# Performance work log

Measured on AMD Instinct MI355X. Metric: run time of the kernel, lower is better.

Reference implementation:

```python
import jax, jax.numpy as jnp
import numpy as np

B, S, D, H = 4, 2048, 512, 8
DK = D // H


def setup_inputs() -> dict:
    key = jax.random.key(0)
    ks = jax.random.split(key, 8)
    std = 1.0 / np.sqrt(D)
    return {
        "query": jax.random.normal(ks[0], (B, S, D), jnp.float32),
        "key": jax.random.normal(ks[1], (B, S, D), jnp.float32),
        "value": jax.random.normal(ks[2], (B, S, D), jnp.float32),
        "Wq": jax.random.normal(ks[3], (D, D), jnp.float32) * std,
        "Wk": jax.random.normal(ks[4], (D, D), jnp.float32) * std,
        "Wv": jax.random.normal(ks[5], (D, D), jnp.float32) * std,
        "Wo": jax.random.normal(ks[6], (D, D), jnp.float32) * std,
        "bo": jnp.zeros((D,), jnp.float32),
    }


def reference(query, key, value, Wq, Wk, Wv, Wo, bo):
    # nn.Linear stores weight [out, in]; y = x @ W.T
    def split_heads(x):  # [B,S,D] -> [B,H,S,DK]
        return x.reshape(B, S, H, DK).transpose(0, 2, 1, 3)

    Q = split_heads(query @ Wq.T)
    K = split_heads(key @ Wk.T)
    V = split_heads(value @ Wv.T)
    scale = jnp.sqrt(jnp.asarray(DK, Q.dtype))
    scores = jnp.einsum("bhqd,bhkd->bhqk", Q, K) / scale  # [B,H,S,S]
    attn = jax.nn.softmax(scores, axis=-1)  # dropout=0 / eval mode
    ctx = jnp.einsum("bhqk,bhkd->bhqd", attn, V)
    ctx = ctx.transpose(0, 2, 1, 3).reshape(B, S, D)
    return ctx @ Wo.T + bo
```

## Files before the change

### kernel.cpp

```cpp
#include <hip/hip_runtime.h>
#include <hip/hip_bf16.h>
#include <stdint.h>

#define DEV __device__ __forceinline__

typedef __attribute__((ext_vector_type(8))) __bf16 bf16x8;
typedef __attribute__((ext_vector_type(4))) float f32x4;
typedef __attribute__((ext_vector_type(16))) float f32x16;
typedef __attribute__((ext_vector_type(4))) short short4v;
typedef __attribute__((ext_vector_type(8))) short short8v;
typedef __attribute__((ext_vector_type(4))) unsigned int uint4v;

constexpr int B_ = 4, S_ = 2048, D_ = 512, H_ = 8, DK_ = 64;
constexpr int M_ = B_ * S_;
constexpr int K_ = D_;

DEV unsigned short f2bf(float f) {
  unsigned int u = __builtin_bit_cast(unsigned int, f);
  unsigned int r = (u + 0x7fffu + ((u >> 16) & 1u)) >> 16;
  return (unsigned short)r;
}

DEV void gld16(const void* g, void* l) {
  __builtin_amdgcn_global_load_lds(
      (const __attribute__((address_space(1))) unsigned int*)g,
      (__attribute__((address_space(3))) unsigned int*)l, 16, 0, 0);
}

DEV f32x4 mfma16(bf16x8 a, bf16x8 b, f32x4 c) {
  return __builtin_amdgcn_mfma_f32_16x16x32_bf16(a, b, c, 0, 0, 0);
}
DEV f32x16 mfma32(bf16x8 a, bf16x8 b, f32x16 c) {
  return __builtin_amdgcn_mfma_f32_32x32x16_bf16(a, b, c, 0, 0, 0);
}

DEV short4v tr16(const void* p) {
  short4v d;
  asm volatile("ds_read_b64_tr_b16 %0, %1"
               : "=v"(d)
               : "v"((const __attribute__((address_space(3))) char*)p));
  return d;
}

DEV unsigned pkbf(float a, float b) {
  unsigned r;
  asm("v_cvt_pk_bf16_f32 %0, %1, %2" : "=v"(r) : "v"(a), "v"(b));
  return r;
}

DEV void pl32swap(unsigned& a, unsigned& b) {
  asm volatile("v_permlane32_swap_b32 %0, %1" : "+v"(a), "+v"(b));
}

__global__ __launch_bounds__(256) void convert_all(
    const float* __restrict__ q, const float* __restrict__ k, const float* __restrict__ v,
    const float* __restrict__ wq, const float* __restrict__ wk,
    const float* __restrict__ wv, const float* __restrict__ wo,
    unsigned short* __restrict__ xq, unsigned short* __restrict__ xk,
    unsigned short* __restrict__ xv, unsigned short* __restrict__ wqb,
    unsigned short* __restrict__ wkb, unsigned short* __restrict__ wvb,
    unsigned short* __restrict__ wob)
{
  constexpr int NX = M_ * D_;
  constexpr int NW = D_ * D_;
  constexpr int TOT = (3 * NX + 4 * NW) / 4;
  for (int u = blockIdx.x * blockDim.x + threadIdx.x; u < TOT;
       u += gridDim.x * blockDim.x) {
    int e = u * 4;
    const float* src; unsigned short* dst; int off;
    if (e < 3 * NX) {
      int t = e >> 22; off = e & (NX - 1);
      src = (t == 0) ? q : ((t == 1) ? k : v);
      dst = (t == 0) ? xq : ((t == 1) ? xk : xv);
    } else {
      int e2 = e - 3 * NX;
      int t = e2 >> 18; off = e2 & (NW - 1);
      src = (t == 0) ? wq : ((t == 1) ? wk : ((t == 2) ? wv : wo));
      dst = (t == 0) ? wqb : ((t == 1) ? wkb : ((t == 2) ? wvb : wob));
    }
    float4 f = *(const float4*)(src + off);
    short4v o;
    o.x = (short)f2bf(f.x); o.y = (short)f2bf(f.y);
    o.z = (short)f2bf(f.z); o.w = (short)f2bf(f.w);
    *(short4v*)(dst + off) = o;
  }
}

template <int MODE>
__global__ __launch_bounds__(256, 2) void gemm_bt(
    const unsigned short* __restrict__ A, const unsigned short* __restrict__ W,
    unsigned short* __restrict__ outH, float* __restrict__ outF,
    const float* __restrict__ bias)
{
  constexpr int BM = 128, BN = 64, BK = 64, NKT = K_ / BK;
  __shared__ unsigned short As[2][BM * BK];
  __shared__ unsigned short Bs[2][BN * BK];
  const int tid = threadIdx.x, lane = tid & 63, wave = tid >> 6;
  const int bn0 = blockIdx.x * BN, bm0 = blockIdx.y * BM;
  const int wr = (wave >> 1) * 64, wc = (wave & 1) * 32;
  const int frow = lane & 15, fk16 = (lane >> 4) * 16;

  f32x4 acc[4][2];
#pragma unroll
  for (int i = 0; i < 4; ++i)
#pragma unroll
    for (int j = 0; j < 2; ++j)
#pragma unroll
      for (int r = 0; r < 4; ++r) acc[i][j][r] = 0.f;

  auto stage = [&](int kt, int buf) {
#pragma unroll
    for (int i = 0; i < 4; ++i) {
      int o = (wave * 4 + i) * 1024;
      int ol = o + lane * 16;
      int src = ol ^ (((ol >> 7) & 7) << 4);
      gld16((const char*)A + (size_t)(bm0 + (src >> 7)) * (K_ * 2) + kt * 128 + (src & 127),
            (char*)As[buf] + o);
    }
#pragma unroll
    for (int i = 0; i < 2; ++i) {
      int o = (wave * 2 + i) * 1024;
      int ol = o + lane * 16;
      int src = ol ^ (((ol >> 7) & 7) << 4);
      gld16((const char*)W + (size_t)(bn0 + (src >> 7)) * (K_ * 2) + kt * 128 + (src & 127),
            (char*)Bs[buf] + o);
    }
  };

  stage(0, 0);
  __syncthreads();
  int cur = 0;
  for (int kt = 0; kt < NKT; ++kt) {
    if (kt + 1 < NKT) stage(kt + 1, cur ^ 1);
#pragma unroll
    for (int kc = 0; kc < 2; ++kc) {
      bf16x8 a[4], b[2];
#pragma unroll
      for (int i = 0; i < 4; ++i) {
        int row = wr + i * 16 + frow;
        a[i] = *(const bf16x8*)((const char*)As[cur] +
                ((row * 128 + kc * 64 + fk16) ^ ((row & 7) << 4)));
      }
#pragma unroll
      for (int j = 0; j < 2; ++j) {
        int row = wc + j * 16 + frow;
        b[j] = *(const bf16x8*)((const char*)Bs[cur] +
                ((row * 128 + kc * 64 + fk16) ^ ((row & 7) << 4)));
      }
      __builtin_amdgcn_s_setprio(1);
#pragma unroll
      for (int i = 0; i < 4; ++i)
#pragma unroll
        for (int j = 0; j < 2; ++j)
          acc[i][j] = mfma16(a[i], b[j], acc[i][j]);
      __builtin_amdgcn_s_setprio(0);
    }
    __syncthreads();
    cur ^= 1;
  }

  const int r0 = (lane >> 4) * 4, cn = lane & 15;
#pragma unroll
  for (int i = 0; i < 4; ++i)
#pragma unroll
    for (int j = 0; j < 2; ++j)
#pragma unroll
      for (int r = 0; r < 4; ++r) {
        int gm = bm0 + wr + i * 16 + r0 + r;
        int gn = bn0 + wc + j * 16 + cn;
        float val = acc[i][j][r];
        if (MODE == 0) {
          int bb = gm >> 11, ss = gm & (S_ - 1), hh = gn >> 6, dk = gn & 63;
          outH[((size_t)(bb * H_ + hh) * S_ + ss) * DK_ + dk] = f2bf(val);
        } else {
          outF[(size_t)gm * D_ + gn] = val + bias[gn];
        }
      }
}

__global__ __launch_bounds__(256, 2) void attn(
    const unsigned short* __restrict__ Qb, const unsigned short* __restrict__ Kb,
    const unsigned short* __restrict__ Vb, unsigned short* __restrict__ Ctx)
{
  constexpr int QB = 128, KVB = 64, NT = S_ / KVB;
  __shared__ unsigned short Qs[QB * DK_];
  __shared__ unsigned short Kd[2][KVB * DK_];
  __shared__ unsigned short Vd[2][KVB * DK_];
  __shared__ float smA[4][32];
  const int tid = threadIdx.x, lane = tid & 63, wave = tid >> 6;
  const int hi = lane >> 5, l31 = lane & 31, g1 = (lane >> 4) & 1;
  const int bh = blockIdx.y, q0 = blockIdx.x * QB;
  const size_t hb = (size_t)bh * S_ * DK_;
  const char* Qg = (const char*)(Qb + hb + (size_t)q0 * DK_);
  const char* Kg = (const char*)(Kb + hb);
  const char* Vg = (const char*)(Vb + hb);

  auto stageSwz = [&](const char* gbase, unsigned short* lds, int o) {
    int ol = o + lane * 16;
    int src = ol ^ (((ol >> 7) & 7) << 4);
    gld16(gbase + src, (char*)lds + o);
  };
  auto stageVt = [&](const char* gbase, unsigned short* lds, int o) {
    int ol = o + lane * 16;
    int E0 = ol >> 1;
    int st = E0 >> 6, rr = (E0 >> 4) & 3, c0 = E0 & 15;
    int kk = (st >> 2) * 4 + rr, dd = (st & 3) * 16 + c0;
    gld16(gbase + (kk * DK_ + dd) * 2, (char*)lds + o);
  };

#pragma unroll
  for (int i = 0; i < 4; ++i) stageSwz(Qg, Qs, (wave * 4 + i) * 1024);
#pragma unroll
  for (int i = 0; i < 2; ++i) stageSwz(Kg, Kd[0], (wave * 2 + i) * 1024);
#pragma unroll
  for (int i = 0; i < 2; ++i) stageVt(Vg, Vd[0], (wave * 2 + i) * 1024);
  __syncthreads();

  bf16x8 qf[4];
  {
    int row = wave * 32 + l31;
    int rb = row * 128, sw = (row & 7) << 4;
#pragma unroll
    for (int c = 0; c < 4; ++c)
      qf[c] = *(const bf16x8*)((const char*)Qs + ((rb + c * 32 + hi * 16) ^ sw));
  }

  f32x16 oacc[2];
#pragma unroll
  for (int dt = 0; dt < 2; ++dt)
#pragma unroll
    for (int r = 0; r < 16; ++r) oacc[dt][r] = 0.f;
  float m2 = -1e30f, lsum = 0.f;
  constexpr float SCL2 = 0.125f * 1.44269504089f;

  int cur = 0;
  for (int t = 0; t < NT; ++t) {
    if (t + 1 < NT) {
      const char* Kg1 = Kg + (size_t)(t + 1) * (KVB * DK_ * 2);
      const char* Vg1 = Vg + (size_t)(t + 1) * (KVB * DK_ * 2);
#pragma unroll
      for (int i = 0; i < 2; ++i) stageSwz(Kg1, Kd[cur ^ 1], (wave * 2 + i) * 1024);
#pragma unroll
      for (int i = 0; i < 2; ++i) stageVt(Vg1, Vd[cur ^ 1], (wave * 2 + i) * 1024);
    }

    f32x16 sacc[2];
#pragma unroll
    for (int k2 = 0; k2 < 2; ++k2)
#pragma unroll
      for (int r = 0; r < 16; ++r) sacc[k2][r] = 0.f;
    __builtin_amdgcn_s_setprio(1);
#pragma unroll
    for (int c = 0; c < 4; ++c) {
#pragma unroll
      for (int k2 = 0; k2 < 2; ++k2) {
        int row = k2 * 32 + l31;
        bf16x8 kf = *(const bf16x8*)((const char*)Kd[cur] +
                     ((row * 128 + c * 32 + hi * 16) ^ ((row & 7) << 4)));
        sacc[k2] = mfma32(kf, qf[c], sacc[k2]);
      }
    }
    __builtin_amdgcn_s_setprio(0);

    float mloc = sacc[0][0];
#pragma unroll
    for (int k2 = 0; k2 < 2; ++k2)
#pragma unroll
      for (int r = 0; r < 16; ++r) mloc = fmaxf(mloc, sacc[k2][r]);
    mloc = fmaxf(mloc, __shfl_xor(mloc, 32));
    float m2n = fmaxf(m2, mloc * SCL2);
    float alpha = __builtin_amdgcn_exp2f(m2 - m2n);
    m2 = m2n;
    float psum = 0.f;
#pragma unroll
    for (int k2 = 0; k2 < 2; ++k2)
#pragma unroll
      for (int r = 0; r < 16; ++r) {
        float p = __builtin_amdgcn_exp2f(fmaf(sacc[k2][r], SCL2, -m2n));
        sacc[k2][r] = p;
        psum += p;
      }
    psum += __shfl_xor(psum, 32);
    lsum = lsum * alpha + psum;

    if (lane < 32) smA[wave][lane] = alpha;
    f32x4 av[4];
#pragma unroll
    for (int s = 0; s < 4; ++s)
      av[s] = *(const f32x4*)&smA[wave][s * 8 + hi * 4];
#pragma unroll
    for (int dt = 0; dt < 2; ++dt)
#pragma unroll
      for (int r = 0; r < 16; ++r) oacc[dt][r] *= av[r >> 2][r & 3];

    short4v va[4][2][2];
#pragma unroll
    for (int c = 0; c < 4; ++c)
#pragma unroll
      for (int dt = 0; dt < 2; ++dt) {
        int st = 16 * c + 8 * hi + 2 * dt + g1;
        const char* ad = (const char*)Vd[cur] + st * 128 + (lane & 15) * 8;
        va[c][dt][0] = tr16(ad);
        va[c][dt][1] = tr16(ad + 512);
      }
    bf16x8 pfrag[4];
#pragma unroll
    for (int c = 0; c < 4; ++c) {
      const f32x16& P = sacc[c >> 1];
      const int b = (c & 1) * 8;
      unsigned d0 = pkbf(P[b + 0], P[b + 1]);
      unsigned d1 = pkbf(P[b + 2], P[b + 3]);
      unsigned d2 = pkbf(P[b + 4], P[b + 5]);
      unsigned d3 = pkbf(P[b + 6], P[b + 7]);
      pl32swap(d0, d2);
      pl32swap(d1, d3);
      uint4v pi = {d0, d1, d2, d3};
      pfrag[c] = __builtin_bit_cast(bf16x8, pi);
    }
    asm volatile("s_waitcnt lgkmcnt(0)" ::: "memory");
    __builtin_amdgcn_sched_barrier(0);
    __builtin_amdgcn_s_setprio(1);
#pragma unroll
    for (int c = 0; c < 4; ++c)
#pragma unroll
      for (int dt = 0; dt < 2; ++dt) {
        short8v vv = __builtin_shufflevector(va[c][dt][0], va[c][dt][1],
                                             0, 1, 2, 3, 4, 5, 6, 7);
        oacc[dt] = mfma32(pfrag[c], __builtin_bit_cast(bf16x8, vv), oacc[dt]);
      }
    __builtin_amdgcn_s_setprio(0);

    __syncthreads();
    cur ^= 1;
  }

  if (lane < 32) smA[wave][lane] = 1.f / lsum;
  f32x4 iv[4];
#pragma unroll
  for (int s = 0; s < 4; ++s)
    iv[s] = *(const f32x4*)&smA[wave][s * 8 + hi * 4];
  const int bq = bh >> 3, hh = bh & 7;
#pragma unroll
  for (int dt = 0; dt < 2; ++dt)
#pragma unroll
    for (int r = 0; r < 16; ++r) {
      int qq = (r & 3) + 8 * (r >> 2) + 4 * hi;
      int grow = q0 + wave * 32 + qq;
      int col = hh * 64 + dt * 32 + l31;
      Ctx[((size_t)bq * S_ + grow) * D_ + col] = f2bf(oacc[dt][r] * iv[r >> 2][r & 3]);
    }
}

extern "C" void kernel_launch(void* const* d_in, const int* in_sizes, int n_in,
                              void* d_out, int out_size, void* d_ws, size_t ws_size,
                              hipStream_t stream) {
  const float* q  = (const float*)d_in[0];
  const float* k  = (const float*)d_in[1];
  const float* v  = (const float*)d_in[2];
  const float* wq = (const float*)d_in[3];
  const float* wk = (const float*)d_in[4];
  const float* wv = (const float*)d_in[5];
  const float* wo = (const float*)d_in[6];
  const float* bo = (const float*)d_in[7];
  float* out = (float*)d_out;

  constexpr size_t NX = (size_t)M_ * D_;
  constexpr size_t NW = (size_t)D_ * D_;
  char* ws = (char*)d_ws;
  unsigned short* Xq  = (unsigned short*)ws; ws += NX * 2;
  unsigned short* Xk  = (unsigned short*)ws; ws += NX * 2;
  unsigned short* Xv  = (unsigned short*)ws; ws += NX * 2;
  unsigned short* Wqb = (unsigned short*)ws; ws += NW * 2;
  unsigned short* Wkb = (unsigned short*)ws; ws += NW * 2;
  unsigned short* Wvb = (unsigned short*)ws; ws += NW * 2;
  unsigned short* Wob = (unsigned short*)ws; ws += NW * 2;
  unsigned short* Qbf = (unsigned short*)ws; ws += NX * 2;
  unsigned short* Kbf = (unsigned short*)ws; ws += NX * 2;
  unsigned short* Vbf = (unsigned short*)ws; ws += NX * 2;
  unsigned short* Cx  = (unsigned short*)ws; ws += NX * 2;

  convert_all<<<2048, 256, 0, stream>>>(q, k, v, wq, wk, wv, wo,
                                        Xq, Xk, Xv, Wqb, Wkb, Wvb, Wob);
  dim3 ggrid(D_ / 64, M_ / 128);
  gemm_bt<0><<<ggrid, 256, 0, stream>>>(Xq, Wqb, Qbf, nullptr, nullptr);
  gemm_bt<0><<<ggrid, 256, 0, stream>>>(Xk, Wkb, Kbf, nullptr, nullptr);
  gemm_bt<0><<<ggrid, 256, 0, stream>>>(Xv, Wvb, Vbf, nullptr, nullptr);
  attn<<<dim3(S_ / 128, B_ * H_), 256, 0, stream>>>(Qbf, Kbf, Vbf, Cx);
  gemm_bt<1><<<ggrid, 256, 0, stream>>>(Cx, Wob, nullptr, out, bo);
}
```

Baseline: 212.8 us.

## Batch QKV projections into one launch, widen GEMM tiles, keep Q/K/V row-major

```diff
diff --git a/kernel.cpp b/kernel.cpp
--- a/kernel.cpp
+++ b/kernel.cpp
@@ -88,41 +88,51 @@
 
 template <int MODE>
 __global__ __launch_bounds__(256, 2) void gemm_bt(
-    const unsigned short* __restrict__ A, const unsigned short* __restrict__ W,
-    unsigned short* __restrict__ outH, float* __restrict__ outF,
-    const float* __restrict__ bias)
+    const unsigned short* __restrict__ A0, const unsigned short* __restrict__ A1,
+    const unsigned short* __restrict__ A2,
+    const unsigned short* __restrict__ W0, const unsigned short* __restrict__ W1,
+    const unsigned short* __restrict__ W2,
+    unsigned short* __restrict__ O0, unsigned short* __restrict__ O1,
+    unsigned short* __restrict__ O2,
+    float* __restrict__ outF, const float* __restrict__ bias)
 {
-  constexpr int BM = 128, BN = 64, BK = 64, NKT = K_ / BK;
+  constexpr int BM = (MODE == 0) ? 128 : 64;
+  constexpr int BN = 128, BK = 64, NKT = K_ / BK;
+  constexpr int AFR = BM / 32;
   __shared__ unsigned short As[2][BM * BK];
   __shared__ unsigned short Bs[2][BN * BK];
   const int tid = threadIdx.x, lane = tid & 63, wave = tid >> 6;
+  const int z = blockIdx.z;
+  const unsigned short* A = (MODE == 1 || z == 0) ? A0 : (z == 1 ? A1 : A2);
+  const unsigned short* W = (MODE == 1 || z == 0) ? W0 : (z == 1 ? W1 : W2);
+  unsigned short* outH = (MODE == 1 || z == 0) ? O0 : (z == 1 ? O1 : O2);
   const int bn0 = blockIdx.x * BN, bm0 = blockIdx.y * BM;
-  const int wr = (wave >> 1) * 64, wc = (wave & 1) * 32;
+  const int wr = (wave >> 1) * (BM / 2), wc = (wave & 1) * 64;
   const int frow = lane & 15, fk16 = (lane >> 4) * 16;
 
-  f32x4 acc[4][2];
-#pragma unroll
-  for (int i = 0; i < 4; ++i)
-#pragma unroll
-    for (int j = 0; j < 2; ++j)
+  f32x4 acc[AFR][4];
+#pragma unroll
+  for (int i = 0; i < AFR; ++i)
+#pragma unroll
+    for (int j = 0; j < 4; ++j)
 #pragma unroll
       for (int r = 0; r < 4; ++r) acc[i][j][r] = 0.f;
 
   auto stage = [&](int kt, int buf) {
+#pragma unroll
+    for (int i = 0; i < BM / 32; ++i) {
+      int o = (wave * (BM / 32) + i) * 1024;
+      int ol = o + lane * 16;
+      int row = ol >> 7, off = (ol ^ ((row & 7) << 4)) & 127;
+      gld16((const char*)A + (size_t)(bm0 + row) * (K_ * 2) + kt * 128 + off,
+            (char*)As[buf] + o);
+    }
 #pragma unroll
     for (int i = 0; i < 4; ++i) {
       int o = (wave * 4 + i) * 1024;
       int ol = o + lane * 16;
-      int src = ol ^ (((ol >> 7) & 7) << 4);
-      gld16((const char*)A + (size_t)(bm0 + (src >> 7)) * (K_ * 2) + kt * 128 + (src & 127),
-            (char*)As[buf] + o);
-    }
-#pragma unroll
-    for (int i = 0; i < 2; ++i) {
-      int o = (wave * 2 + i) * 1024;
-      int ol = o + lane * 16;
-      int src = ol ^ (((ol >> 7) & 7) << 4);
-      gld16((const char*)W + (size_t)(bn0 + (src >> 7)) * (K_ * 2) + kt * 128 + (src & 127),
+      int row = ol >> 7, off = (ol ^ ((row & 7) << 4)) & 127;
+      gld16((const char*)W + (size_t)(bn0 + row) * (K_ * 2) + kt * 128 + off,
             (char*)Bs[buf] + o);
     }
   };
@@ -134,24 +144,24 @@
     if (kt + 1 < NKT) stage(kt + 1, cur ^ 1);
 #pragma unroll
     for (int kc = 0; kc < 2; ++kc) {
-      bf16x8 a[4], b[2];
-#pragma unroll
-      for (int i = 0; i < 4; ++i) {
+      bf16x8 a[AFR], b[4];
+#pragma unroll
+      for (int i = 0; i < AFR; ++i) {
         int row = wr + i * 16 + frow;
         a[i] = *(const bf16x8*)((const char*)As[cur] +
                 ((row * 128 + kc * 64 + fk16) ^ ((row & 7) << 4)));
       }
 #pragma unroll
-      for (int j = 0; j < 2; ++j) {
+      for (int j = 0; j < 4; ++j) {
         int row = wc + j * 16 + frow;
         b[j] = *(const bf16x8*)((const char*)Bs[cur] +
                 ((row * 128 + kc * 64 + fk16) ^ ((row & 7) << 4)));
       }
       __builtin_amdgcn_s_setprio(1);
 #pragma unroll
-      for (int i = 0; i < 4; ++i)
-#pragma unroll
-        for (int j = 0; j < 2; ++j)
+      for (int i = 0; i < AFR; ++i)
+#pragma unroll
+        for (int j = 0; j < 4; ++j)
           acc[i][j] = mfma16(a[i], b[j], acc[i][j]);
       __builtin_amdgcn_s_setprio(0);
     }
@@ -160,27 +170,28 @@
   }
 
   const int r0 = (lane >> 4) * 4, cn = lane & 15;
-#pragma unroll
-  for (int i = 0; i < 4; ++i)
-#pragma unroll
-    for (int j = 0; j < 2; ++j)
+  float bv[4];
+  if (MODE == 1) {
+#pragma unroll
+    for (int j = 0; j < 4; ++j) bv[j] = bias[bn0 + wc + j * 16 + cn];
+  }
+#pragma unroll
+  for (int i = 0; i < AFR; ++i)
+#pragma unroll
+    for (int j = 0; j < 4; ++j)
 #pragma unroll
       for (int r = 0; r < 4; ++r) {
         int gm = bm0 + wr + i * 16 + r0 + r;
         int gn = bn0 + wc + j * 16 + cn;
         float val = acc[i][j][r];
-        if (MODE == 0) {
-          int bb = gm >> 11, ss = gm & (S_ - 1), hh = gn >> 6, dk = gn & 63;
-          outH[((size_t)(bb * H_ + hh) * S_ + ss) * DK_ + dk] = f2bf(val);
-        } else {
-          outF[(size_t)gm * D_ + gn] = val + bias[gn];
-        }
+        if (MODE == 0) outH[(size_t)gm * D_ + gn] = f2bf(val);
+        else           outF[(size_t)gm * D_ + gn] = val + bv[j];
       }
 }
 
 __global__ __launch_bounds__(256, 2) void attn(
-    const unsigned short* __restrict__ Qb, const unsigned short* __restrict__ Kb,
-    const unsigned short* __restrict__ Vb, unsigned short* __restrict__ Ctx)
+    const unsigned short* __restrict__ Qm, const unsigned short* __restrict__ Km,
+    const unsigned short* __restrict__ Vm, unsigned short* __restrict__ Ctx)
 {
   constexpr int QB = 128, KVB = 64, NT = S_ / KVB;
   __shared__ unsigned short Qs[QB * DK_];
@@ -190,22 +201,22 @@
   const int tid = threadIdx.x, lane = tid & 63, wave = tid >> 6;
   const int hi = lane >> 5, l31 = lane & 31, g1 = (lane >> 4) & 1;
   const int bh = blockIdx.y, q0 = blockIdx.x * QB;
-  const size_t hb = (size_t)bh * S_ * DK_;
-  const char* Qg = (const char*)(Qb + hb + (size_t)q0 * DK_);
-  const char* Kg = (const char*)(Kb + hb);
-  const char* Vg = (const char*)(Vb + hb);
+  const int bq = bh >> 3, hh = bh & 7;
+  const char* Qg = (const char*)(Qm + ((size_t)bq * S_ + q0) * D_ + hh * DK_);
+  const char* Kg = (const char*)(Km + (size_t)bq * S_ * D_ + hh * DK_);
+  const char* Vg = (const char*)(Vm + (size_t)bq * S_ * D_ + hh * DK_);
 
   auto stageSwz = [&](const char* gbase, unsigned short* lds, int o) {
     int ol = o + lane * 16;
-    int src = ol ^ (((ol >> 7) & 7) << 4);
-    gld16(gbase + src, (char*)lds + o);
+    int row = ol >> 7, off = (ol ^ ((row & 7) << 4)) & 127;
+    gld16(gbase + (size_t)row * 1024 + off, (char*)lds + o);
   };
   auto stageVt = [&](const char* gbase, unsigned short* lds, int o) {
     int ol = o + lane * 16;
     int E0 = ol >> 1;
     int st = E0 >> 6, rr = (E0 >> 4) & 3, c0 = E0 & 15;
     int kk = (st >> 2) * 4 + rr, dd = (st & 3) * 16 + c0;
-    gld16(gbase + (kk * DK_ + dd) * 2, (char*)lds + o);
+    gld16(gbase + (size_t)kk * 1024 + dd * 2, (char*)lds + o);
   };
 
 #pragma unroll
@@ -236,8 +247,8 @@
   int cur = 0;
   for (int t = 0; t < NT; ++t) {
     if (t + 1 < NT) {
-      const char* Kg1 = Kg + (size_t)(t + 1) * (KVB * DK_ * 2);
-      const char* Vg1 = Vg + (size_t)(t + 1) * (KVB * DK_ * 2);
+      const char* Kg1 = Kg + (size_t)(t + 1) * KVB * 1024;
+      const char* Vg1 = Vg + (size_t)(t + 1) * KVB * 1024;
 #pragma unroll
       for (int i = 0; i < 2; ++i) stageSwz(Kg1, Kd[cur ^ 1], (wave * 2 + i) * 1024);
 #pragma unroll
@@ -339,7 +350,6 @@
 #pragma unroll
   for (int s = 0; s < 4; ++s)
     iv[s] = *(const f32x4*)&smA[wave][s * 8 + hi * 4];
-  const int bq = bh >> 3, hh = bh & 7;
 #pragma unroll
   for (int dt = 0; dt < 2; ++dt)
 #pragma unroll
@@ -381,10 +391,10 @@
 
   convert_all<<<2048, 256, 0, stream>>>(q, k, v, wq, wk, wv, wo,
                                         Xq, Xk, Xv, Wqb, Wkb, Wvb, Wob);
-  dim3 ggrid(D_ / 64, M_ / 128);
-  gemm_bt<0><<<ggrid, 256, 0, stream>>>(Xq, Wqb, Qbf, nullptr, nullptr);
-  gemm_bt<0><<<ggrid, 256, 0, stream>>>(Xk, Wkb, Kbf, nullptr, nullptr);
-  gemm_bt<0><<<ggrid, 256, 0, stream>>>(Xv, Wvb, Vbf, nullptr, nullptr);
+  gemm_bt<0><<<dim3(4, 64, 3), 256, 0, stream>>>(
+      Xq, Xk, Xv, Wqb, Wkb, Wvb, Qbf, Kbf, Vbf, nullptr, nullptr);
   attn<<<dim3(S_ / 128, B_ * H_), 256, 0, stream>>>(Qbf, Kbf, Vbf, Cx);
-  gemm_bt<1><<<ggrid, 256, 0, stream>>>(Cx, Wob, nullptr, out, bo);
-}
+  gemm_bt<1><<<dim3(4, 128, 1), 256, 0, stream>>>(
+      Cx, nullptr, nullptr, Wob, nullptr, nullptr, nullptr, nullptr, nullptr,
+      out, bo);
+}
```

After: 201.9 us. -5.1%, faster.
